# Kernel tuning notes

Hardware: AMD Instinct MI355X
Metric: run time of the kernel (lower is better)

The kernel has to match this reference:

```python
import jax, jax.numpy as jnp
import numpy as np

S = 16        # each mode size of the TT shape (16,16,16,16)
R = 4         # bond dimension
B = 1024      # batch
INIT_STD = 0.05  # keras 'random_normal' initializer stddev


def setup_inputs() -> dict:
    key = jax.random.key(0)
    ks = jax.random.split(key, 6)
    x = jax.random.normal(ks[0], (B, S * S * S * S), dtype=jnp.float32)
    # TT cores, per build(): core_1 (S,S,R); middle cores (S,S,R,R); last core (S,S,R)
    G1 = INIT_STD * jax.random.normal(ks[1], (S, S, R), dtype=jnp.float32)
    G2 = INIT_STD * jax.random.normal(ks[2], (S, S, R, R), dtype=jnp.float32)
    G3 = INIT_STD * jax.random.normal(ks[3], (S, S, R, R), dtype=jnp.float32)
    G4 = INIT_STD * jax.random.normal(ks[4], (S, S, R), dtype=jnp.float32)
    bias = jnp.zeros((S, S, S, S), dtype=jnp.float32)  # tf.zeros(shape=self.shape)
    return {"x": x, "G1": G1, "G2": G2, "G3": G3, "G4": G4, "bias": bias}


def reference(x, G1, G2, G3, G4, bias):
    # Per sample: reshape to (S,S,S,S) and contract the TT chain (ncon network):
    # out[a,b,c,d] = sum_{i,j,k,l,r,s,t} x[i,j,k,l] G1[a,i,r] G2[b,j,r,s] G3[c,k,s,t] G4[d,l,t]
    n = x.shape[0]
    xr = x.reshape(n, S, S, S, S)
    out = jnp.einsum('nijkl,air,bjrs,ckst,dlt->nabcd', xr, G1, G2, G3, G4,
                     optimize=True)
    out = out + bias  # broadcast bias over batch
    return jax.nn.relu(out.reshape(n, S * S * S * S))
```

## Files before the change

kernel.cpp:

```cpp
#include <hip/hip_runtime.h>
#include <hip/hip_bf16.h>


typedef __attribute__((ext_vector_type(8))) short bf16x8;
typedef __attribute__((ext_vector_type(4))) float f32x4;
typedef unsigned short u16;
typedef unsigned long long u64;

#define T2_PER_N 262144
#define PAD40 40
#define PAD72 72


static __device__ __forceinline__ u16 f2bf(float f) {
  __hip_bfloat16 h = __float2bfloat16(f);
  return *reinterpret_cast<u16*>(&h);
}
static __device__ __forceinline__ u64 pack4(f32x4 a) {
  union { u16 s[4]; u64 u; } p;
  p.s[0] = f2bf(a[0]); p.s[1] = f2bf(a[1]); p.s[2] = f2bf(a[2]); p.s[3] = f2bf(a[3]);
  return p.u;
}
#define MFMA(A, B, C) __builtin_amdgcn_mfma_f32_16x16x32_bf16((A), (B), (C), 0, 0, 0)

__global__ void tt_prep(const float* __restrict__ G1, const float* __restrict__ G2,
                        const float* __restrict__ G3, const float* __restrict__ G4,
                        u16* __restrict__ img)
{
  const int tid = threadIdx.x;
  const uint4 z = {0, 0, 0, 0};
  for (int idx = tid; idx < 1616; idx += 256) ((uint4*)img)[idx] = z;
  __syncthreads();
  #pragma unroll
  for (int it = 0; it < 4; ++it) {
    const int e = it * 256 + tid, a = e >> 6, i = (e >> 2) & 15, r = e & 3;
    img[(a * 4 + r) * PAD40 + i] = f2bf(G1[e]);
  }
  #pragma unroll
  for (int it = 0; it < 16; ++it) {
    const int e = it * 256 + tid, b = e >> 8, j = (e >> 4) & 15, r = (e >> 2) & 3, s = e & 3;
    img[2560 + (b * 4 + s) * PAD72 + j * 4 + r] = f2bf(G2[e]);
  }
  #pragma unroll
  for (int it = 0; it < 16; ++it) {
    const int e = it * 256 + tid, c = e >> 8, k = (e >> 4) & 15, s = (e >> 2) & 3, t = e & 3;
    img[7168 + (c * 4 + t) * PAD72 + k * 4 + s] = f2bf(G3[e]);
  }
  #pragma unroll
  for (int it = 0; it < 4; ++it) {
    const int e = it * 256 + tid, d = e >> 6, l = (e >> 2) & 15, t = e & 3;
    img[11776 + d * PAD72 + t * 16 + l] = f2bf(G4[e]);
  }
}

__global__ __launch_bounds__(512, 4) void tt_passA(
    const float* __restrict__ x, const u16* __restrict__ img,
    u16* __restrict__ T2, int n0)
{
  const int tid = threadIdx.x;
  const int kp   = blockIdx.x;
  const int slot = blockIdx.y;
  const int n = n0 + slot;
  const int lane = tid & 63, w = tid >> 6, quad = (lane >> 4) & 3, ln = lane & 15;

  __shared__ __align__(16) u16 gAs[7168];
  __shared__ __align__(16) u16 xs [256 * PAD40];
  __shared__ __align__(16) u16 t1s[256 * PAD72];

  for (int idx = tid; idx < 896; idx += 512)
    ((uint4*)gAs)[idx] = ((const uint4*)img)[idx];
  {
    const uint4 z = {0, 0, 0, 0};
    const int row = tid >> 1, h = tid & 1;
    *(uint4*)&xs[row * PAD40 + 16 + h * 8] = z;
  }

  const float4* xg = (const float4*)x + (size_t)n * 16384;
  uint4* Tg = (uint4*)(T2 + (size_t)slot * T2_PER_N);

  #pragma unroll
  for (int kx = 0; kx < 2; ++kx) {
    const int k = kp * 2 + kx;
    #pragma unroll
    for (int it = 0; it < 2; ++it) {
      const int e = it * 512 + tid, i = (e >> 2) & 15, j = e >> 6, lq = e & 3;
      const float4 v = xg[i * 1024 + j * 64 + k * 4 + lq];
      xs[(j * 16 + lq * 4 + 0) * PAD40 + i] = f2bf(v.x);
      xs[(j * 16 + lq * 4 + 1) * PAD40 + i] = f2bf(v.y);
      xs[(j * 16 + lq * 4 + 2) * PAD40 + i] = f2bf(v.z);
      xs[(j * 16 + lq * 4 + 3) * PAD40 + i] = f2bf(v.w);
    }
    __syncthreads();

    {
      bf16x8 a1[2];
      #pragma unroll
      for (int t = 0; t < 2; ++t)
        a1[t] = *(const bf16x8*)&xs[((w * 2 + t) * 16 + ln) * PAD40 + quad * 8];
      #pragma unroll
      for (int tn = 0; tn < 4; ++tn) {
        const bf16x8 b1 = *(const bf16x8*)&gAs[(tn * 16 + ln) * PAD40 + quad * 8];
        #pragma unroll
        for (int t = 0; t < 2; ++t) {
          f32x4 acc = {0.f, 0.f, 0.f, 0.f};
          acc = MFMA(b1, a1[t], acc);
          *(u64*)&t1s[((tn * 4 + quad) * 16 + ln) * PAD72 + (w * 2 + t) * 4] = pack4(acc);
        }
      }
    }
    __syncthreads();

    {
      bf16x8 a2[2][2];
      #pragma unroll
      for (int t = 0; t < 2; ++t)
        #pragma unroll
        for (int ks = 0; ks < 2; ++ks)
          a2[t][ks] = *(const bf16x8*)&t1s[((w * 2 + t) * 16 + ln) * PAD72 + ks * 32 + quad * 8];
      __syncthreads();
      const u16* g2s = gAs + 2560;
      #pragma unroll
      for (int tn = 0; tn < 4; ++tn) {
        const bf16x8 b20 = *(const bf16x8*)&g2s[(tn * 16 + ln) * PAD72 + quad * 8];
        const bf16x8 b21 = *(const bf16x8*)&g2s[(tn * 16 + ln) * PAD72 + 32 + quad * 8];
        #pragma unroll
        for (int t = 0; t < 2; ++t) {
          f32x4 acc = {0.f, 0.f, 0.f, 0.f};
          acc = MFMA(b20, a2[t][0], acc);
          acc = MFMA(b21, a2[t][1], acc);
          *(u64*)&t1s[((w * 2 + t) * 16 + ln) * PAD72 + tn * 16 + quad * 4] = pack4(acc);
        }
      }
    }
    __syncthreads();

    #pragma unroll
    for (int it = 0; it < 4; ++it) {
      const int e = it * 512 + tid, row = e >> 3, seg = e & 7;
      const uint4 q = *(const uint4*)&t1s[row * PAD72 + seg * 8];
      Tg[(row >> 4) * 2048 + k * 128 + (row & 15) * 8 + seg] = q;
    }
  }
}

__global__ __launch_bounds__(512, 4) void tt_passB(
    const u16* __restrict__ T2, const u16* __restrict__ img,
    const float* __restrict__ bias, float* __restrict__ out, int n0)
{
  const int tid = threadIdx.x;
  const int a    = blockIdx.x;
  const int slot = blockIdx.y;
  const int n = n0 + slot;
  const int lane = tid & 63, w = tid >> 6, quad = (lane >> 4) & 3, ln = lane & 15;

  __shared__ __align__(16) u16 gBs[5760];
  __shared__ __align__(16) u16 t2a[256 * PAD72];

  for (int idx = tid; idx < 720; idx += 512)
    ((uint4*)gBs)[idx] = ((const uint4*)(img + 7168))[idx];
  {
    const uint4* Tg = (const uint4*)(T2 + (size_t)slot * T2_PER_N) + a * 2048;
    #pragma unroll
    for (int it = 0; it < 4; ++it) {
      const int e = it * 512 + tid, kl = e >> 3, bq = e & 7;
      const uint4 q = Tg[e];
      const int k = kl >> 4, l = kl & 15, b0 = bq * 2;
      const u64 lo = ((u64)q.y << 32) | q.x, hi = ((u64)q.w << 32) | q.z;
      *(u64*)&t2a[(b0 * 16 + l) * PAD72 + k * 4]       = lo;
      *(u64*)&t2a[((b0 + 1) * 16 + l) * PAD72 + k * 4] = hi;
    }
  }
  __syncthreads();

  {
    bf16x8 a3[2][2];
    #pragma unroll
    for (int t = 0; t < 2; ++t)
      #pragma unroll
      for (int ks = 0; ks < 2; ++ks)
        a3[t][ks] = *(const bf16x8*)&t2a[((w * 2 + t) * 16 + ln) * PAD72 + ks * 32 + quad * 8];
    __syncthreads();
    #pragma unroll
    for (int tn = 0; tn < 4; ++tn) {
      const bf16x8 b30 = *(const bf16x8*)&gBs[(tn * 16 + ln) * PAD72 + quad * 8];
      const bf16x8 b31 = *(const bf16x8*)&gBs[(tn * 16 + ln) * PAD72 + 32 + quad * 8];
      #pragma unroll
      for (int t = 0; t < 2; ++t) {
        f32x4 acc = {0.f, 0.f, 0.f, 0.f};
        acc = MFMA(a3[t][0], b30, acc);
        acc = MFMA(a3[t][1], b31, acc);
        *(u64*)&t2a[((w * 2 + t) * 16 + tn * 4 + (ln >> 2)) * PAD72 + (ln & 3) * 16 + quad * 4]
            = pack4(acc);
      }
    }
  }
  __syncthreads();

  {
    const u16* g4s = gBs + 4608;
    bf16x8 b4[2];
    #pragma unroll
    for (int ks = 0; ks < 2; ++ks)
      b4[ks] = *(const bf16x8*)&g4s[ln * PAD72 + ks * 32 + quad * 8];
    const size_t obase = (size_t)n * 65536;
    #pragma unroll
    for (int t = 0; t < 2; ++t) {
      bf16x8 a40 = *(const bf16x8*)&t2a[((w * 2 + t) * 16 + ln) * PAD72 + quad * 8];
      bf16x8 a41 = *(const bf16x8*)&t2a[((w * 2 + t) * 16 + ln) * PAD72 + 32 + quad * 8];
      f32x4 acc = {0.f, 0.f, 0.f, 0.f};
      acc = MFMA(a40, b4[0], acc);
      acc = MFMA(a41, b4[1], acc);
      #pragma unroll
      for (int r = 0; r < 4; ++r) {
        const int m4 = (w * 2 + t) * 16 + quad * 4 + r;
        const int off = a * 4096 + m4 * 16 + ln;
        const float v = acc[r] + bias[off];
        out[obase + off] = fmaxf(v, 0.f);
      }
    }
  }
}

extern "C" void kernel_launch(void* const* d_in, const int* in_sizes, int n_in,
                              void* d_out, int out_size, void* d_ws, size_t ws_size,
                              hipStream_t stream) {
  const float* x    = (const float*)d_in[0];
  const float* G1   = (const float*)d_in[1];
  const float* G2   = (const float*)d_in[2];
  const float* G3   = (const float*)d_in[3];
  const float* G4   = (const float*)d_in[4];
  const float* bias = (const float*)d_in[5];
  float* out = (float*)d_out;
  u16* img = (u16*)d_ws;
  u16* T2  = (u16*)d_ws + 16384;

  const int Bn = 1024;
  const size_t per_n = (size_t)T2_PER_N * sizeof(u16);
  size_t avail = (ws_size > 32768) ? (ws_size - 32768) : 0;
  int chunk = (int)(avail / per_n);
  if (chunk > 256) chunk = 256;
  if (chunk < 1) chunk = 1;

  tt_prep<<<1, 256, 0, stream>>>(G1, G2, G3, G4, img);
  for (int nn0 = 0; nn0 < Bn; nn0 += chunk) {
    const int c = (nn0 + chunk <= Bn) ? chunk : (Bn - nn0);
    tt_passA<<<dim3(8, c), 512, 0, stream>>>(x, img, T2, nn0);
    tt_passB<<<dim3(16, c), 512, 0, stream>>>(T2, img, bias, out, nn0);
  }
}
```

Baseline: 639.0 us.

## Pre-convert x to swizzled bf16 and load tiles via global_load_lds

```diff
diff --git a/kernel.cpp b/kernel.cpp
--- a/kernel.cpp
+++ b/kernel.cpp
@@ -21,6 +21,11 @@
   p.s[0] = f2bf(a[0]); p.s[1] = f2bf(a[1]); p.s[2] = f2bf(a[2]); p.s[3] = f2bf(a[3]);
   return p.u;
 }
+static __device__ __forceinline__ void gload_lds16(const void* g, void* l) {
+  __builtin_amdgcn_global_load_lds(
+      (const __attribute__((address_space(1))) unsigned int*)g,
+      (__attribute__((address_space(3))) unsigned int*)l, 16, 0, 0);
+}
 #define MFMA(A, B, C) __builtin_amdgcn_mfma_f32_16x16x32_bf16((A), (B), (C), 0, 0, 0)
 
 __global__ void tt_prep(const float* __restrict__ G1, const float* __restrict__ G2,
@@ -53,8 +58,38 @@
   }
 }
 
+__global__ __launch_bounds__(256, 4) void tt_prep_x(const float* __restrict__ x,
+                                                    u16* __restrict__ xb)
+{
+  const int tid = threadIdx.x;
+  const int kq = blockIdx.x;
+  const int n  = blockIdx.y;
+  __shared__ __align__(16) u16 im[4 * 4112];
+  const int lane = tid & 63, wv = tid >> 6;
+  const int j2 = lane >> 4, kk = (lane >> 2) & 3, lq = lane & 3;
+  const float4* xg = (const float4*)x + (size_t)n * 16384;
+  const int j = wv * 4 + j2, k = kq * 4 + kk;
+  #pragma unroll
+  for (int i = 0; i < 16; ++i) {
+    const float4 v = xg[i * 1024 + j * 64 + k * 4 + lq];
+    const int sb = (i >> 3) ^ (lq & 1);
+    const int base = kk * 4112 + (j * 16 + lq * 4) * 16 + sb * 8 + (i & 7);
+    im[base]      = f2bf(v.x);
+    im[base + 16] = f2bf(v.y);
+    im[base + 32] = f2bf(v.z);
+    im[base + 48] = f2bf(v.w);
+  }
+  __syncthreads();
+  uint4* xo = (uint4*)(xb + (size_t)n * 65536 + (size_t)kq * 16384);
+  #pragma unroll
+  for (int it = 0; it < 8; ++it) {
+    const int e = it * 256 + tid, kk2 = e >> 9, off = e & 511;
+    xo[e] = *(const uint4*)&im[kk2 * 4112 + off * 8];
+  }
+}
+
 __global__ __launch_bounds__(512, 4) void tt_passA(
-    const float* __restrict__ x, const u16* __restrict__ img,
+    const u16* __restrict__ xb, const u16* __restrict__ img,
     u16* __restrict__ T2, int n0)
 {
   const int tid = threadIdx.x;
@@ -64,39 +99,31 @@
   const int lane = tid & 63, w = tid >> 6, quad = (lane >> 4) & 3, ln = lane & 15;
 
   __shared__ __align__(16) u16 gAs[7168];
-  __shared__ __align__(16) u16 xs [256 * PAD40];
+  __shared__ __align__(16) u16 xs [2 * 4096];
   __shared__ __align__(16) u16 t1s[256 * PAD72];
 
-  for (int idx = tid; idx < 896; idx += 512)
-    ((uint4*)gAs)[idx] = ((const uint4*)img)[idx];
-  {
-    const uint4 z = {0, 0, 0, 0};
-    const int row = tid >> 1, h = tid & 1;
-    *(uint4*)&xs[row * PAD40 + 16 + h * 8] = z;
-  }
-
-  const float4* xg = (const float4*)x + (size_t)n * 16384;
-  uint4* Tg = (uint4*)(T2 + (size_t)slot * T2_PER_N);
+  for (int c = w; c < 14; c += 8)
+    gload_lds16(img + c * 512 + lane * 8, &gAs[c * 512]);
+  const u16* xbn = xb + (size_t)n * 65536;
+  #pragma unroll
+  for (int kx = 0; kx < 2; ++kx)
+    gload_lds16(xbn + (kp * 2 + kx) * 4096 + w * 512 + lane * 8, &xs[kx * 4096 + w * 512]);
+  asm volatile("s_waitcnt vmcnt(0)" ::: "memory");
+  __syncthreads();
+
+  u64* Tg = (u64*)(T2 + (size_t)slot * T2_PER_N);
+  const int sb = (quad & 1) ^ ((ln >> 2) & 1);
 
   #pragma unroll
   for (int kx = 0; kx < 2; ++kx) {
     const int k = kp * 2 + kx;
-    #pragma unroll
-    for (int it = 0; it < 2; ++it) {
-      const int e = it * 512 + tid, i = (e >> 2) & 15, j = e >> 6, lq = e & 3;
-      const float4 v = xg[i * 1024 + j * 64 + k * 4 + lq];
-      xs[(j * 16 + lq * 4 + 0) * PAD40 + i] = f2bf(v.x);
-      xs[(j * 16 + lq * 4 + 1) * PAD40 + i] = f2bf(v.y);
-      xs[(j * 16 + lq * 4 + 2) * PAD40 + i] = f2bf(v.z);
-      xs[(j * 16 + lq * 4 + 3) * PAD40 + i] = f2bf(v.w);
-    }
-    __syncthreads();
+    if (kx) __syncthreads();
 
     {
       bf16x8 a1[2];
       #pragma unroll
       for (int t = 0; t < 2; ++t)
-        a1[t] = *(const bf16x8*)&xs[((w * 2 + t) * 16 + ln) * PAD40 + quad * 8];
+        a1[t] = *(const bf16x8*)&xs[kx * 4096 + ((w * 2 + t) * 16 + ln) * 16 + sb * 8];
       #pragma unroll
       for (int tn = 0; tn < 4; ++tn) {
         const bf16x8 b1 = *(const bf16x8*)&gAs[(tn * 16 + ln) * PAD40 + quad * 8];
@@ -117,7 +144,6 @@
         #pragma unroll
         for (int ks = 0; ks < 2; ++ks)
           a2[t][ks] = *(const bf16x8*)&t1s[((w * 2 + t) * 16 + ln) * PAD72 + ks * 32 + quad * 8];
-      __syncthreads();
       const u16* g2s = gAs + 2560;
       #pragma unroll
       for (int tn = 0; tn < 4; ++tn) {
@@ -128,17 +154,10 @@
           f32x4 acc = {0.f, 0.f, 0.f, 0.f};
           acc = MFMA(b20, a2[t][0], acc);
           acc = MFMA(b21, a2[t][1], acc);
-          *(u64*)&t1s[((w * 2 + t) * 16 + ln) * PAD72 + tn * 16 + quad * 4] = pack4(acc);
+          const int a = w * 2 + t;
+          Tg[(a * 16384 + (k * 16 + ln) * 64 + tn * 16 + quad * 4) >> 2] = pack4(acc);
         }
       }
-    }
-    __syncthreads();
-
-    #pragma unroll
-    for (int it = 0; it < 4; ++it) {
-      const int e = it * 512 + tid, row = e >> 3, seg = e & 7;
-      const uint4 q = *(const uint4*)&t1s[row * PAD72 + seg * 8];
-      Tg[(row >> 4) * 2048 + k * 128 + (row & 15) * 8 + seg] = q;
     }
   }
 }
@@ -153,11 +172,15 @@
   const int n = n0 + slot;
   const int lane = tid & 63, w = tid >> 6, quad = (lane >> 4) & 3, ln = lane & 15;
 
-  __shared__ __align__(16) u16 gBs[5760];
+  __shared__ __align__(16) u16 g3s[4608];
   __shared__ __align__(16) u16 t2a[256 * PAD72];
 
-  for (int idx = tid; idx < 720; idx += 512)
-    ((uint4*)gBs)[idx] = ((const uint4*)(img + 7168))[idx];
+  for (int c = w; c < 9; c += 8)
+    gload_lds16(img + 7168 + c * 512 + lane * 8, &g3s[c * 512]);
+  bf16x8 b4[2];
+  #pragma unroll
+  for (int ks = 0; ks < 2; ++ks)
+    b4[ks] = *(const bf16x8*)&img[11776 + ln * PAD72 + ks * 32 + quad * 8];
   {
     const uint4* Tg = (const uint4*)(T2 + (size_t)slot * T2_PER_N) + a * 2048;
     #pragma unroll
@@ -170,6 +193,7 @@
       *(u64*)&t2a[((b0 + 1) * 16 + l) * PAD72 + k * 4] = hi;
     }
   }
+  asm volatile("s_waitcnt vmcnt(0)" ::: "memory");
   __syncthreads();
 
   {
@@ -182,8 +206,8 @@
     __syncthreads();
     #pragma unroll
     for (int tn = 0; tn < 4; ++tn) {
-      const bf16x8 b30 = *(const bf16x8*)&gBs[(tn * 16 + ln) * PAD72 + quad * 8];
-      const bf16x8 b31 = *(const bf16x8*)&gBs[(tn * 16 + ln) * PAD72 + 32 + quad * 8];
+      const bf16x8 b30 = *(const bf16x8*)&g3s[(tn * 16 + ln) * PAD72 + quad * 8];
+      const bf16x8 b31 = *(const bf16x8*)&g3s[(tn * 16 + ln) * PAD72 + 32 + quad * 8];
       #pragma unroll
       for (int t = 0; t < 2; ++t) {
         f32x4 acc = {0.f, 0.f, 0.f, 0.f};
@@ -197,11 +221,6 @@
   __syncthreads();
 
   {
-    const u16* g4s = gBs + 4608;
-    bf16x8 b4[2];
-    #pragma unroll
-    for (int ks = 0; ks < 2; ++ks)
-      b4[ks] = *(const bf16x8*)&g4s[ln * PAD72 + ks * 32 + quad * 8];
     const size_t obase = (size_t)n * 65536;
     #pragma unroll
     for (int t = 0; t < 2; ++t) {
@@ -232,19 +251,22 @@
   const float* bias = (const float*)d_in[5];
   float* out = (float*)d_out;
   u16* img = (u16*)d_ws;
-  u16* T2  = (u16*)d_ws + 16384;
+  u16* xb  = img + 16384;
+  u16* T2  = xb + (size_t)1024 * 65536;
 
   const int Bn = 1024;
+  const size_t head = 32768 + (size_t)1024 * 131072;
   const size_t per_n = (size_t)T2_PER_N * sizeof(u16);
-  size_t avail = (ws_size > 32768) ? (ws_size - 32768) : 0;
+  size_t avail = (ws_size > head) ? (ws_size - head) : 0;
   int chunk = (int)(avail / per_n);
   if (chunk > 256) chunk = 256;
   if (chunk < 1) chunk = 1;
 
   tt_prep<<<1, 256, 0, stream>>>(G1, G2, G3, G4, img);
+  tt_prep_x<<<dim3(4, 1024), 256, 0, stream>>>(x, xb);
   for (int nn0 = 0; nn0 < Bn; nn0 += chunk) {
     const int c = (nn0 + chunk <= Bn) ? chunk : (Bn - nn0);
-    tt_passA<<<dim3(8, c), 512, 0, stream>>>(x, img, T2, nn0);
+    tt_passA<<<dim3(8, c), 512, 0, stream>>>(xb, img, T2, nn0);
     tt_passB<<<dim3(16, c), 512, 0, stream>>>(T2, img, bias, out, nn0);
   }
 }
```

Measured after the change: 741.6 us. +16.1%, slower.

## Process several samples per block with register-prefetched global loads in both passes

Applied to the files above, without the earlier changes.

```diff
diff --git a/kernel.cpp b/kernel.cpp
--- a/kernel.cpp
+++ b/kernel.cpp
@@ -55,12 +55,11 @@
 
 __global__ __launch_bounds__(512, 4) void tt_passA(
     const float* __restrict__ x, const u16* __restrict__ img,
-    u16* __restrict__ T2, int n0)
+    u16* __restrict__ T2, int n0, int nper)
 {
   const int tid = threadIdx.x;
-  const int kp   = blockIdx.x;
-  const int slot = blockIdx.y;
-  const int n = n0 + slot;
+  const int kp  = blockIdx.x;
+  const int sb  = blockIdx.y * nper;
   const int lane = tid & 63, w = tid >> 6, quad = (lane >> 4) & 3, ln = lane & 15;
 
   __shared__ __align__(16) u16 gAs[7168];
@@ -75,21 +74,33 @@
     *(uint4*)&xs[row * PAD40 + 16 + h * 8] = z;
   }
 
-  const float4* xg = (const float4*)x + (size_t)n * 16384;
-  uint4* Tg = (uint4*)(T2 + (size_t)slot * T2_PER_N);
-
-  #pragma unroll
-  for (int kx = 0; kx < 2; ++kx) {
-    const int k = kp * 2 + kx;
-    #pragma unroll
-    for (int it = 0; it < 2; ++it) {
-      const int e = it * 512 + tid, i = (e >> 2) & 15, j = e >> 6, lq = e & 3;
-      const float4 v = xg[i * 1024 + j * 64 + k * 4 + lq];
-      xs[(j * 16 + lq * 4 + 0) * PAD40 + i] = f2bf(v.x);
-      xs[(j * 16 + lq * 4 + 1) * PAD40 + i] = f2bf(v.y);
-      xs[(j * 16 + lq * 4 + 2) * PAD40 + i] = f2bf(v.z);
-      xs[(j * 16 + lq * 4 + 3) * PAD40 + i] = f2bf(v.w);
-    }
+  const int lq = tid & 3, i = (tid >> 2) & 15, j0 = tid >> 6;
+  const size_t xoff0 = (size_t)i * 1024 + j0 * 64 + lq;
+  const size_t xoff1 = xoff0 + 8 * 64;
+  const int r0 = (j0 * 16 + lq * 4) * PAD40 + i;
+  const int r1 = ((j0 + 8) * 16 + lq * 4) * PAD40 + i;
+
+  const float4* xg0 = (const float4*)x + (size_t)(n0 + sb) * 16384;
+  float4 p0 = xg0[xoff0 + kp * 8];
+  float4 p1 = xg0[xoff1 + kp * 8];
+
+  for (int it = 0; it < 2 * nper; ++it) {
+    const int sm = it >> 1, kx = it & 1, k = kp * 2 + kx;
+    const float4 c0 = p0, c1 = p1;
+    if (it + 1 < 2 * nper) {
+      const int sm2 = (it + 1) >> 1, k2 = kp * 2 + ((it + 1) & 1);
+      const float4* xg2 = (const float4*)x + (size_t)(n0 + sb + sm2) * 16384;
+      p0 = xg2[xoff0 + k2 * 4];
+      p1 = xg2[xoff1 + k2 * 4];
+    }
+    xs[r0]             = f2bf(c0.x);
+    xs[r0 + PAD40]     = f2bf(c0.y);
+    xs[r0 + 2 * PAD40] = f2bf(c0.z);
+    xs[r0 + 3 * PAD40] = f2bf(c0.w);
+    xs[r1]             = f2bf(c1.x);
+    xs[r1 + PAD40]     = f2bf(c1.y);
+    xs[r1 + 2 * PAD40] = f2bf(c1.z);
+    xs[r1 + 3 * PAD40] = f2bf(c1.w);
     __syncthreads();
 
     {
@@ -134,88 +145,112 @@
     }
     __syncthreads();
 
-    #pragma unroll
-    for (int it = 0; it < 4; ++it) {
-      const int e = it * 512 + tid, row = e >> 3, seg = e & 7;
-      const uint4 q = *(const uint4*)&t1s[row * PAD72 + seg * 8];
-      Tg[(row >> 4) * 2048 + k * 128 + (row & 15) * 8 + seg] = q;
+    {
+      uint4* Tg = (uint4*)(T2 + (size_t)(sb + sm) * T2_PER_N);
+      #pragma unroll
+      for (int s4 = 0; s4 < 4; ++s4) {
+        const int e = s4 * 512 + tid, row = e >> 3, seg = e & 7;
+        const uint4 q = *(const uint4*)&t1s[row * PAD72 + seg * 8];
+        Tg[(row >> 4) * 2048 + k * 128 + (row & 15) * 8 + seg] = q;
+      }
     }
   }
 }
 
 __global__ __launch_bounds__(512, 4) void tt_passB(
     const u16* __restrict__ T2, const u16* __restrict__ img,
-    const float* __restrict__ bias, float* __restrict__ out, int n0)
+    const float* __restrict__ bias, float* __restrict__ out, int n0, int nper)
 {
   const int tid = threadIdx.x;
-  const int a    = blockIdx.x;
-  const int slot = blockIdx.y;
-  const int n = n0 + slot;
+  const int a   = blockIdx.x;
+  const int sb  = blockIdx.y * nper;
   const int lane = tid & 63, w = tid >> 6, quad = (lane >> 4) & 3, ln = lane & 15;
 
-  __shared__ __align__(16) u16 gBs[5760];
+  __shared__ __align__(16) u16 g3s[4608];
   __shared__ __align__(16) u16 t2a[256 * PAD72];
 
-  for (int idx = tid; idx < 720; idx += 512)
-    ((uint4*)gBs)[idx] = ((const uint4*)(img + 7168))[idx];
+  for (int idx = tid; idx < 576; idx += 512)
+    ((uint4*)g3s)[idx] = ((const uint4*)(img + 7168))[idx];
+  bf16x8 b4[2];
+  #pragma unroll
+  for (int ks = 0; ks < 2; ++ks)
+    b4[ks] = *(const bf16x8*)&img[11776 + ln * PAD72 + ks * 32 + quad * 8];
+  float brg[2][4];
+  #pragma unroll
+  for (int t = 0; t < 2; ++t)
+    #pragma unroll
+    for (int r = 0; r < 4; ++r)
+      brg[t][r] = bias[a * 4096 + ((w * 2 + t) * 16 + quad * 4 + r) * 16 + ln];
+
+  uint4 p0, p1, p2, p3;
   {
-    const uint4* Tg = (const uint4*)(T2 + (size_t)slot * T2_PER_N) + a * 2048;
-    #pragma unroll
-    for (int it = 0; it < 4; ++it) {
-      const int e = it * 512 + tid, kl = e >> 3, bq = e & 7;
-      const uint4 q = Tg[e];
-      const int k = kl >> 4, l = kl & 15, b0 = bq * 2;
-      const u64 lo = ((u64)q.y << 32) | q.x, hi = ((u64)q.w << 32) | q.z;
-      *(u64*)&t2a[(b0 * 16 + l) * PAD72 + k * 4]       = lo;
-      *(u64*)&t2a[((b0 + 1) * 16 + l) * PAD72 + k * 4] = hi;
-    }
-  }
-  __syncthreads();
-
-  {
-    bf16x8 a3[2][2];
-    #pragma unroll
-    for (int t = 0; t < 2; ++t)
-      #pragma unroll
-      for (int ks = 0; ks < 2; ++ks)
-        a3[t][ks] = *(const bf16x8*)&t2a[((w * 2 + t) * 16 + ln) * PAD72 + ks * 32 + quad * 8];
-    __syncthreads();
-    #pragma unroll
-    for (int tn = 0; tn < 4; ++tn) {
-      const bf16x8 b30 = *(const bf16x8*)&gBs[(tn * 16 + ln) * PAD72 + quad * 8];
-      const bf16x8 b31 = *(const bf16x8*)&gBs[(tn * 16 + ln) * PAD72 + 32 + quad * 8];
+    const uint4* Tg = (const uint4*)(T2 + (size_t)sb * T2_PER_N) + a * 2048;
+    p0 = Tg[tid]; p1 = Tg[512 + tid]; p2 = Tg[1024 + tid]; p3 = Tg[1536 + tid];
+  }
+
+  for (int itn = 0; itn < nper; ++itn) {
+    const int slot = sb + itn;
+    const uint4 c0 = p0, c1 = p1, c2 = p2, c3 = p3;
+    if (itn + 1 < nper) {
+      const uint4* Tg = (const uint4*)(T2 + (size_t)(slot + 1) * T2_PER_N) + a * 2048;
+      p0 = Tg[tid]; p1 = Tg[512 + tid]; p2 = Tg[1024 + tid]; p3 = Tg[1536 + tid];
+    }
+    if (itn) __syncthreads();
+
+    {
+      const uint4 cc[4] = {c0, c1, c2, c3};
+      #pragma unroll
+      for (int s4 = 0; s4 < 4; ++s4) {
+        const int e = s4 * 512 + tid, kl = e >> 3, bq = e & 7;
+        const uint4 q = cc[s4];
+        const int k = kl >> 4, l = kl & 15, b0 = bq * 2;
+        const u64 lo = ((u64)q.y << 32) | q.x, hi = ((u64)q.w << 32) | q.z;
+        *(u64*)&t2a[(b0 * 16 + l) * PAD72 + k * 4]       = lo;
+        *(u64*)&t2a[((b0 + 1) * 16 + l) * PAD72 + k * 4] = hi;
+      }
+    }
+    __syncthreads();
+
+    {
+      bf16x8 a3[2][2];
+      #pragma unroll
+      for (int t = 0; t < 2; ++t)
+        #pragma unroll
+        for (int ks = 0; ks < 2; ++ks)
+          a3[t][ks] = *(const bf16x8*)&t2a[((w * 2 + t) * 16 + ln) * PAD72 + ks * 32 + quad * 8];
+      __syncthreads();
+      #pragma unroll
+      for (int tn = 0; tn < 4; ++tn) {
+        const bf16x8 b30 = *(const bf16x8*)&g3s[(tn * 16 + ln) * PAD72 + quad * 8];
+        const bf16x8 b31 = *(const bf16x8*)&g3s[(tn * 16 + ln) * PAD72 + 32 + quad * 8];
+        #pragma unroll
+        for (int t = 0; t < 2; ++t) {
+          f32x4 acc = {0.f, 0.f, 0.f, 0.f};
+          acc = MFMA(a3[t][0], b30, acc);
+          acc = MFMA(a3[t][1], b31, acc);
+          *(u64*)&t2a[((w * 2 + t) * 16 + tn * 4 + (ln >> 2)) * PAD72 + (ln & 3) * 16 + quad * 4]
+              = pack4(acc);
+        }
+      }
+    }
+    __syncthreads();
+
+    {
+      const size_t obase = (size_t)(n0 + slot) * 65536;
       #pragma unroll
       for (int t = 0; t < 2; ++t) {
+        bf16x8 a40 = *(const bf16x8*)&t2a[((w * 2 + t) * 16 + ln) * PAD72 + quad * 8];
+        bf16x8 a41 = *(const bf16x8*)&t2a[((w * 2 + t) * 16 + ln) * PAD72 + 32 + quad * 8];
         f32x4 acc = {0.f, 0.f, 0.f, 0.f};
-        acc = MFMA(a3[t][0], b30, acc);
-        acc = MFMA(a3[t][1], b31, acc);
-        *(u64*)&t2a[((w * 2 + t) * 16 + tn * 4 + (ln >> 2)) * PAD72 + (ln & 3) * 16 + quad * 4]
-            = pack4(acc);
-      }
-    }
-  }
-  __syncthreads();
-
-  {
-    const u16* g4s = gBs + 4608;
-    bf16x8 b4[2];
-    #pragma unroll
-    for (int ks = 0; ks < 2; ++ks)
-      b4[ks] = *(const bf16x8*)&g4s[ln * PAD72 + ks * 32 + quad * 8];
-    const size_t obase = (size_t)n * 65536;
-    #pragma unroll
-    for (int t = 0; t < 2; ++t) {
-      bf16x8 a40 = *(const bf16x8*)&t2a[((w * 2 + t) * 16 + ln) * PAD72 + quad * 8];
-      bf16x8 a41 = *(const bf16x8*)&t2a[((w * 2 + t) * 16 + ln) * PAD72 + 32 + quad * 8];
-      f32x4 acc = {0.f, 0.f, 0.f, 0.f};
-      acc = MFMA(a40, b4[0], acc);
-      acc = MFMA(a41, b4[1], acc);
-      #pragma unroll
-      for (int r = 0; r < 4; ++r) {
-        const int m4 = (w * 2 + t) * 16 + quad * 4 + r;
-        const int off = a * 4096 + m4 * 16 + ln;
-        const float v = acc[r] + bias[off];
-        out[obase + off] = fmaxf(v, 0.f);
+        acc = MFMA(a40, b4[0], acc);
+        acc = MFMA(a41, b4[1], acc);
+        #pragma unroll
+        for (int r = 0; r < 4; ++r) {
+          const int m4 = (w * 2 + t) * 16 + quad * 4 + r;
+          const int off = a * 4096 + m4 * 16 + ln;
+          const float v = acc[r] + brg[t][r];
+          out[obase + off] = fmaxf(v, 0.f);
+        }
       }
     }
   }
@@ -239,12 +274,14 @@
   size_t avail = (ws_size > 32768) ? (ws_size - 32768) : 0;
   int chunk = (int)(avail / per_n);
   if (chunk > 256) chunk = 256;
-  if (chunk < 1) chunk = 1;
+  int nsa = 4, nsb = 8;
+  if (chunk >= 8) chunk &= ~7;
+  else { nsa = 1; nsb = 1; if (chunk < 1) chunk = 1; }
 
   tt_prep<<<1, 256, 0, stream>>>(G1, G2, G3, G4, img);
   for (int nn0 = 0; nn0 < Bn; nn0 += chunk) {
     const int c = (nn0 + chunk <= Bn) ? chunk : (Bn - nn0);
-    tt_passA<<<dim3(8, c), 512, 0, stream>>>(x, img, T2, nn0);
-    tt_passB<<<dim3(16, c), 512, 0, stream>>>(T2, img, bias, out, nn0);
-  }
-}
+    tt_passA<<<dim3(8, (c + nsa - 1) / nsa), 512, 0, stream>>>(x, img, T2, nn0, nsa);
+    tt_passB<<<dim3(16, (c + nsb - 1) / nsb), 512, 0, stream>>>(T2, img, bias, out, nn0, nsb);
+  }
+}
```

Result: slower. 658.1 us (+3.0%).

## Prefetch x loads, pack bf16 pairs, write T2 directly from MFMA results

Applied to the files above, without the earlier changes.

```diff
diff --git a/kernel.cpp b/kernel.cpp
--- a/kernel.cpp
+++ b/kernel.cpp
@@ -5,6 +5,7 @@
 typedef __attribute__((ext_vector_type(8))) short bf16x8;
 typedef __attribute__((ext_vector_type(4))) float f32x4;
 typedef unsigned short u16;
+typedef unsigned int u32;
 typedef unsigned long long u64;
 
 #define T2_PER_N 262144
@@ -15,6 +16,9 @@
 static __device__ __forceinline__ u16 f2bf(float f) {
   __hip_bfloat16 h = __float2bfloat16(f);
   return *reinterpret_cast<u16*>(&h);
+}
+static __device__ __forceinline__ u32 bfpair(float a, float b) {
+  return (u32)f2bf(a) | ((u32)f2bf(b) << 16);
 }
 static __device__ __forceinline__ u64 pack4(f32x4 a) {
   union { u16 s[4]; u64 u; } p;
@@ -75,21 +79,29 @@
     *(uint4*)&xs[row * PAD40 + 16 + h * 8] = z;
   }
 
+  const int lq = tid & 3, ip = (tid >> 2) & 7, j = tid >> 5;
+  const size_t xoff0 = (size_t)(2 * ip) * 1024 + j * 64 + lq;
+  const size_t xoff1 = xoff0 + 1024;
+  const int rb = (j * 16 + lq * 4) * PAD40 + 2 * ip;
+
   const float4* xg = (const float4*)x + (size_t)n * 16384;
-  uint4* Tg = (uint4*)(T2 + (size_t)slot * T2_PER_N);
+  float4 p0 = xg[xoff0 + kp * 8];
+  float4 p1 = xg[xoff1 + kp * 8];
+
+  u64* Tg = (u64*)(T2 + (size_t)slot * T2_PER_N);
 
   #pragma unroll
   for (int kx = 0; kx < 2; ++kx) {
     const int k = kp * 2 + kx;
-    #pragma unroll
-    for (int it = 0; it < 2; ++it) {
-      const int e = it * 512 + tid, i = (e >> 2) & 15, j = e >> 6, lq = e & 3;
-      const float4 v = xg[i * 1024 + j * 64 + k * 4 + lq];
-      xs[(j * 16 + lq * 4 + 0) * PAD40 + i] = f2bf(v.x);
-      xs[(j * 16 + lq * 4 + 1) * PAD40 + i] = f2bf(v.y);
-      xs[(j * 16 + lq * 4 + 2) * PAD40 + i] = f2bf(v.z);
-      xs[(j * 16 + lq * 4 + 3) * PAD40 + i] = f2bf(v.w);
-    }
+    const float4 c0 = p0, c1 = p1;
+    if (kx == 0) {
+      p0 = xg[xoff0 + kp * 8 + 4];
+      p1 = xg[xoff1 + kp * 8 + 4];
+    }
+    *(u32*)&xs[rb]             = bfpair(c0.x, c1.x);
+    *(u32*)&xs[rb + PAD40]     = bfpair(c0.y, c1.y);
+    *(u32*)&xs[rb + 2 * PAD40] = bfpair(c0.z, c1.z);
+    *(u32*)&xs[rb + 3 * PAD40] = bfpair(c0.w, c1.w);
     __syncthreads();
 
     {
@@ -117,7 +129,6 @@
         #pragma unroll
         for (int ks = 0; ks < 2; ++ks)
           a2[t][ks] = *(const bf16x8*)&t1s[((w * 2 + t) * 16 + ln) * PAD72 + ks * 32 + quad * 8];
-      __syncthreads();
       const u16* g2s = gAs + 2560;
       #pragma unroll
       for (int tn = 0; tn < 4; ++tn) {
@@ -128,17 +139,10 @@
           f32x4 acc = {0.f, 0.f, 0.f, 0.f};
           acc = MFMA(b20, a2[t][0], acc);
           acc = MFMA(b21, a2[t][1], acc);
-          *(u64*)&t1s[((w * 2 + t) * 16 + ln) * PAD72 + tn * 16 + quad * 4] = pack4(acc);
+          const int arow = w * 2 + t;
+          Tg[(arow * 16384 + (k * 16 + ln) * 64 + tn * 16 + quad * 4) >> 2] = pack4(acc);
         }
       }
-    }
-    __syncthreads();
-
-    #pragma unroll
-    for (int it = 0; it < 4; ++it) {
-      const int e = it * 512 + tid, row = e >> 3, seg = e & 7;
-      const uint4 q = *(const uint4*)&t1s[row * PAD72 + seg * 8];
-      Tg[(row >> 4) * 2048 + k * 128 + (row & 15) * 8 + seg] = q;
     }
   }
 }
```

Measured after the change: 689.8 us. 8.0% more time.
